# Optimization experiments

Hardware: AMD Instinct MI355X
Metric: run time of the kernel (lower is better)

Reference implementation:

```python
import jax, jax.numpy as jnp
import numpy as np

HIDDEN = 768
NUM_BLOCKS = 8
BLOCK = HIDDEN // NUM_BLOCKS  # 96
FACTOR = 1
LAMBDA = 0.01  # sparsity_threshold
HTF = 1.0      # hard_thresholding_fraction
SCALE = 0.02


def setup_inputs() -> dict:
    key = jax.random.key(0)
    kx, k1, k2, k3, k4 = jax.random.split(key, 5)
    B, H, W = 2, 256, 256
    x = jax.random.normal(kx, (B, HIDDEN, H, W), dtype=jnp.float32)
    w1 = SCALE * jax.random.normal(k1, (NUM_BLOCKS, BLOCK, BLOCK * FACTOR, 2), dtype=jnp.float32)
    b1 = SCALE * jax.random.normal(k2, (NUM_BLOCKS, BLOCK * FACTOR, 1, 1, 2), dtype=jnp.float32)
    w2 = SCALE * jax.random.normal(k3, (NUM_BLOCKS, BLOCK * FACTOR, BLOCK, 2), dtype=jnp.float32)
    b2 = SCALE * jax.random.normal(k4, (NUM_BLOCKS, BLOCK, 1, 1, 2), dtype=jnp.float32)
    return {"x": x, "w1": w1, "b1": b1, "w2": w2, "b2": b2}


def _compl_mul_add(a, w, c):
    # a: (b,k,i,x,y,2) real/imag pairs; w: (k,i,o,2); c: (k,o,1,1,2)
    ar, ai = a[..., 0], a[..., 1]
    wr, wi = w[..., 0], w[..., 1]
    rr = jnp.einsum('bkixy,kio->bkoxy', ar, wr)
    ii = jnp.einsum('bkixy,kio->bkoxy', ai, wi)
    ir = jnp.einsum('bkixy,kio->bkoxy', ai, wr)
    ri = jnp.einsum('bkixy,kio->bkoxy', ar, wi)
    return jnp.stack([rr - ii, ir + ri], axis=-1) + c


def _softshrink(x, lam):
    return jnp.where(x > lam, x - lam, jnp.where(x < -lam, x + lam, jnp.zeros_like(x)))


def reference(x, w1, b1, w2, b2):
    B, C, H, W = x.shape
    total_modes = H // 2 + 1
    kept = int(total_modes * HTF)
    bias = x
    xf = jnp.fft.rfft2(x, s=(H, W), axes=(-2, -1), norm='ortho')  # (B,C,H,W//2+1)
    xf = xf.reshape(B, NUM_BLOCKS, BLOCK, H, W // 2 + 1)
    xr = jnp.stack([jnp.real(xf), jnp.imag(xf)], axis=-1)  # view_as_real
    lo, hi = total_modes - kept, total_modes + kept
    o1 = jax.nn.relu(_compl_mul_add(xr[:, :, :, lo:hi, :kept, :], w1, b1))
    o2 = jnp.zeros_like(xr).at[:, :, :, lo:hi, :kept, :].set(_compl_mul_add(o1, w2, b2))
    s = _softshrink(o2, LAMBDA)
    xc = (s[..., 0] + 1j * s[..., 1]).reshape(B, C, H, W // 2 + 1)
    out = jnp.fft.irfft2(xc, s=(H, W), axes=(-2, -1), norm='ortho').astype(x.dtype)
    return out + bias
```

## Files before the change

kernel.cpp:

```cpp
#include <hip/hip_runtime.h>
#include <hip/hip_bf16.h>
#include <math.h>


#define LAMBDA_SS 0.01f

typedef unsigned int u32;
typedef __attribute__((ext_vector_type(8))) short bf16x8;
typedef __attribute__((ext_vector_type(4))) float f32x4;

__device__ __forceinline__ u32 pack_bf16(float r, float i) {
  union { float f; u32 u; } ur, ui;
  ur.f = r; ui.f = i;
  u32 rb = (ur.u + 0x7FFFu + ((ur.u >> 16) & 1u)) >> 16;
  u32 ib = (ui.u + 0x7FFFu + ((ui.u >> 16) & 1u)) >> 16;
  return (ib << 16) | (rb & 0xFFFFu);
}

__device__ __forceinline__ float2 unpack_bf16(u32 p) {
  union { u32 u; float f; } a, b;
  a.u = (p & 0xFFFFu) << 16;
  b.u = (p & 0xFFFF0000u);
  return make_float2(a.f, b.f);
}

__device__ __forceinline__ float sshrink(float v) {
  return (v > LAMBDA_SS) ? v - LAMBDA_SS : ((v < -LAMBDA_SS) ? v + LAMBDA_SS : 0.f);
}

__device__ __forceinline__ float2 cadd(float2 a, float2 b){ return make_float2(a.x+b.x, a.y+b.y); }
__device__ __forceinline__ float2 csub(float2 a, float2 b){ return make_float2(a.x-b.x, a.y-b.y); }
__device__ __forceinline__ float2 cmul(float2 a, float2 b){
  return make_float2(fmaf(a.x,b.x,-a.y*b.y), fmaf(a.x,b.y,a.y*b.x));
}
__device__ __forceinline__ float2 cmulj(float2 a, float si){
  return make_float2(-si*a.y, si*a.x);
}
__device__ __forceinline__ float2 shflx(float2 v, int m){
  return make_float2(__shfl_xor(v.x, m, 64), __shfl_xor(v.y, m, 64));
}
__device__ __forceinline__ float2 shfll(float2 v, int l){
  return make_float2(__shfl(v.x, l, 64), __shfl(v.y, l, 64));
}
__device__ __forceinline__ int brev6(int x){ return (int)(__brev((u32)x) >> 26); }

struct Tw { float2 t128, t64, t32, t16, t8, t4; float si; };

__device__ __forceinline__ float2 mkTw(int e, float si){
  float a = (float)e * 0.0245436926f;
  return make_float2(cosf(a), si*sinf(a));
}
__device__ __forceinline__ Tw make_tw(int lane, float si){
  Tw w; w.si = si;
  w.t128 = mkTw(lane, si);
  w.t64  = mkTw(2*lane, si);
  w.t32  = mkTw((lane&31)*4, si);
  w.t16  = mkTw((lane&15)*8, si);
  w.t8   = mkTw((lane&7)*16, si);
  w.t4   = mkTw((lane&3)*32, si);
  return w;
}

__device__ __forceinline__ float2 bfly_dif(float2 v, int h, float2 th, int lane){
  float2 p = shflx(v, h);
  float sx = (lane & h) ? -1.f : 1.f;
  float2 s = make_float2(fmaf(sx, v.x, p.x), fmaf(sx, v.y, p.y));
  if (lane & h) s = cmul(s, th);
  return s;
}
__device__ __forceinline__ float2 bfly_dit(float2 v, int h, float2 th, int lane){
  if (lane & h) v = cmul(v, th);
  float2 p = shflx(v, h);
  float sx = (lane & h) ? -1.f : 1.f;
  return make_float2(fmaf(sx, v.x, p.x), fmaf(sx, v.y, p.y));
}

__device__ __forceinline__ void fft256_dif(float2 v[4], int lane, const Tw& T){
  float2 t128b = cmulj(T.t128, T.si);
  { float2 a=v[0], b=v[2]; v[0]=cadd(a,b); v[2]=cmul(csub(a,b), T.t128);
    float2 c=v[1], d=v[3]; v[1]=cadd(c,d); v[3]=cmul(csub(c,d), t128b); }
  { float2 a=v[0], b=v[1]; v[0]=cadd(a,b); v[1]=cmul(csub(a,b), T.t64);
    float2 c=v[2], d=v[3]; v[2]=cadd(c,d); v[3]=cmul(csub(c,d), T.t64); }
#pragma unroll
  for (int r=0;r<4;++r) v[r]=bfly_dif(v[r],32,T.t32,lane);
#pragma unroll
  for (int r=0;r<4;++r) v[r]=bfly_dif(v[r],16,T.t16,lane);
#pragma unroll
  for (int r=0;r<4;++r) v[r]=bfly_dif(v[r],8,T.t8,lane);
#pragma unroll
  for (int r=0;r<4;++r) v[r]=bfly_dif(v[r],4,T.t4,lane);
#pragma unroll
  for (int r=0;r<4;++r){
    float2 p=shflx(v[r],2);
    float sx=(lane&2)?-1.f:1.f;
    float2 s=make_float2(fmaf(sx,v[r].x,p.x), fmaf(sx,v[r].y,p.y));
    if ((lane&3)==3) s=cmulj(s,T.si);
    v[r]=s;
  }
#pragma unroll
  for (int r=0;r<4;++r){
    float2 p=shflx(v[r],1);
    float sx=(lane&1)?-1.f:1.f;
    v[r]=make_float2(fmaf(sx,v[r].x,p.x), fmaf(sx,v[r].y,p.y));
  }
}

__device__ __forceinline__ void fft256_dit(float2 v[4], int lane, const Tw& T){
#pragma unroll
  for (int r=0;r<4;++r){
    float2 p=shflx(v[r],1);
    float sx=(lane&1)?-1.f:1.f;
    v[r]=make_float2(fmaf(sx,v[r].x,p.x), fmaf(sx,v[r].y,p.y));
  }
#pragma unroll
  for (int r=0;r<4;++r){
    float2 w=v[r];
    if ((lane&3)==3) w=cmulj(w,T.si);
    float2 p=shflx(w,2);
    float sx=(lane&2)?-1.f:1.f;
    v[r]=make_float2(fmaf(sx,w.x,p.x), fmaf(sx,w.y,p.y));
  }
#pragma unroll
  for (int r=0;r<4;++r) v[r]=bfly_dit(v[r],4,T.t4,lane);
#pragma unroll
  for (int r=0;r<4;++r) v[r]=bfly_dit(v[r],8,T.t8,lane);
#pragma unroll
  for (int r=0;r<4;++r) v[r]=bfly_dit(v[r],16,T.t16,lane);
#pragma unroll
  for (int r=0;r<4;++r) v[r]=bfly_dit(v[r],32,T.t32,lane);
  { v[1]=cmul(v[1],T.t64); float2 a=v[0]; v[0]=cadd(a,v[1]); v[1]=csub(a,v[1]);
    v[3]=cmul(v[3],T.t64); float2 c=v[2]; v[2]=cadd(c,v[3]); v[3]=csub(c,v[3]); }
  { v[2]=cmul(v[2],T.t128); v[3]=cmul(v[3], cmulj(T.t128,T.si));
    float2 a=v[0]; v[0]=cadd(a,v[2]); v[2]=csub(a,v[2]);
    float2 b=v[1]; v[1]=cadd(b,v[3]); v[3]=csub(b,v[3]); }
}

__device__ __forceinline__ int stage_row(int kw){ return 33*(kw&3) + (kw>>2); }

__global__ __launch_bounds__(256) void k_rowfft(const float* __restrict__ x, u32* __restrict__ F) {
  __shared__ u32 stage[131*65];
  const int bc = blockIdx.x >> 2, hc = blockIdx.x & 3;
  const int tid = threadIdx.x, wave = tid >> 6, lane = tid & 63;
  Tw T = make_tw(lane, -1.f);
  const int L = brev6(lane);
  const int laneP0 = brev6((64 - L) & 63);
  const int lanePX = 63 - lane;

  for (int rr = 0; rr < 8; ++rr) {
    const int hl0 = wave*16 + rr*2, hl1 = hl0 + 1;
    const float* xa = x + ((size_t)bc*256 + hc*64 + hl0) * 256;
    float2 v[4];
#pragma unroll
    for (int r=0;r<4;++r){ int d = lane + 64*r; v[r] = make_float2(xa[d], xa[256+d]); }
    fft256_dif(v, lane, T);
#define UNSCR(R, RP, C, LP) { \
      float2 z = v[R]; float2 p = shfll(v[RP], LP); \
      float2 A  = make_float2(0.5f*(z.x+p.x), 0.5f*(z.y-p.y)); \
      float2 Bv = make_float2(0.5f*(z.y+p.y), 0.5f*(p.x-z.x)); \
      int kw = 4*L + (C); \
      if (kw <= 128) { int row = stage_row(kw); \
        stage[row*65 + hl0] = pack_bf16(A.x, A.y); \
        stage[row*65 + hl1] = pack_bf16(Bv.x, Bv.y); } }
    UNSCR(0, 0, 0, laneP0)
    UNSCR(1, 1, 2, lanePX)
    UNSCR(2, 3, 1, lanePX)
    UNSCR(3, 2, 3, lanePX)
#undef UNSCR
  }
  __syncthreads();
  for (int idx = tid; idx < 129*64; idx += 256) {
    int kw = idx >> 6, hl = idx & 63;
    F[((size_t)bc*129 + kw)*256 + hc*64 + hl] = stage[stage_row(kw)*65 + hl];
  }
}

__global__ __launch_bounds__(256) void k_colfft(u32* __restrict__ F, int inverse) {
  const int tid = threadIdx.x, wave = tid >> 6, lane = tid & 63;
  const float si = inverse ? 1.f : -1.f;
  Tw T = make_tw(lane, si);
  u32* p = F + ((size_t)blockIdx.x*4 + wave) * 256;
  float2 v[4];
#pragma unroll
  for (int r=0;r<4;++r) v[r] = unpack_bf16(p[lane + 64*r]);
  if (!inverse) fft256_dif(v, lane, T);
  else          fft256_dit(v, lane, T);
  const float s = 1.0f/256.0f;
#pragma unroll
  for (int r=0;r<4;++r) p[lane + 64*r] = pack_bf16(v[r].x*s, v[r].y*s);
}

__global__ __launch_bounds__(256) void k_prep_w(const float2* __restrict__ w1,
                                                const float2* __restrict__ w2,
                                                u32* __restrict__ Wt) {
  const int blk = blockIdx.x;
  const int k = blk >> 1, layer = blk & 1;
  const float2* w = (layer == 0 ? w1 : w2) + (size_t)k * 96 * 96;
  u32* out = Wt + (size_t)blk * 18432;
  for (int idx = threadIdx.x; idx < 9216; idx += 256) {
    int o = idx % 96, i = idx / 96;
    float2 v = w[i * 96 + o];
    out[(2 * o) * 96 + i]     = pack_bf16(v.x, -v.y);
    out[(2 * o + 1) * 96 + i] = pack_bf16(v.y, v.x);
  }
}

#define MIX_LDS_BYTES (73728 + 49152)

__global__ __launch_bounds__(512) void k_mix_mfma(u32* __restrict__ F,
    const u32* __restrict__ Wt,
    const float2* __restrict__ b1, const float2* __restrict__ b2) {
  extern __shared__ char smem[];
  char* Wlds = smem;
  char* Dlds = smem + 73728;

  const int bi = blockIdx.x;
  const int hc = bi & 1;
  const int kw = (bi >> 1) % 129;
  const int bk = (bi >> 1) / 129;
  const int k = bk & 7, b = bk >> 3;
  const int t = threadIdx.x;
  const int lane = t & 63, wave = t >> 6;
  const int wm = wave >> 2, wn = wave & 3;
  const int lrow = lane & 15;
  const int lk = (lane >> 4) * 16;

  const u32* W1g = Wt + (size_t)(k * 2 + 0) * 18432;
  const u32* W2g = Wt + (size_t)(k * 2 + 1) * 18432;

#pragma unroll
  for (int c = 0; c < 9; ++c) {
    int idx = c * 512 + t;
    int byte = idx * 16;
    int row = idx / 24;
    uint4 v = reinterpret_cast<const uint4*>(W1g)[idx];
    *reinterpret_cast<uint4*>(Wlds + (byte ^ ((row & 7) << 4))) = v;
  }

  const size_t chstride = 129 * 256;
  const size_t base = (((size_t)(b * 768 + k * 96)) * 129 + kw) * 256 + (size_t)hc * 128;
  {
    const int h = t & 127;
    const int pg = t >> 7;
#pragma unroll
    for (int it = 0; it < 12; ++it) {
      int p = it * 4 + pg;
      u32 a0 = F[base + (size_t)(2 * p) * chstride + h];
      u32 a1 = F[base + (size_t)(2 * p + 1) * chstride + h];
      int byte = h * 384 + p * 8;
      *reinterpret_cast<uint2*>(Dlds + (byte ^ ((h & 7) << 4))) = make_uint2(a0, a1);
    }
  }

  uint4 w2buf[9];
#pragma unroll
  for (int c = 0; c < 9; ++c) w2buf[c] = reinterpret_cast<const uint4*>(W2g)[c * 512 + t];

  __syncthreads();

  f32x4 acc[6][2];
#pragma unroll
  for (int mi = 0; mi < 6; ++mi)
#pragma unroll
    for (int ni = 0; ni < 2; ++ni) acc[mi][ni] = (f32x4)0.f;

#pragma unroll
  for (int ks = 0; ks < 6; ++ks) {
    const int kb = ks * 64;
    bf16x8 afrag[6];
#pragma unroll
    for (int mi = 0; mi < 6; ++mi) {
      int row = wm * 96 + mi * 16 + lrow;
      int byte = row * 384 + kb + lk;
      afrag[mi] = *reinterpret_cast<bf16x8*>(Wlds + (byte ^ ((row & 7) << 4)));
    }
#pragma unroll
    for (int ni = 0; ni < 2; ++ni) {
      int row = wn * 32 + ni * 16 + lrow;
      int byte = row * 384 + kb + lk;
      bf16x8 bfrag = *reinterpret_cast<bf16x8*>(Dlds + (byte ^ ((row & 7) << 4)));
#pragma unroll
      for (int mi = 0; mi < 6; ++mi)
        acc[mi][ni] = __builtin_amdgcn_mfma_f32_16x16x32_bf16(afrag[mi], bfrag, acc[mi][ni], 0, 0, 0);
    }
  }
  __syncthreads();

#pragma unroll
  for (int c = 0; c < 9; ++c) {
    int idx = c * 512 + t;
    int byte = idx * 16;
    int row = idx / 24;
    *reinterpret_cast<uint4*>(Wlds + (byte ^ ((row & 7) << 4))) = w2buf[c];
  }
  const float2* b1k = b1 + k * 96;
#pragma unroll
  for (int mi = 0; mi < 6; ++mi) {
    int m0 = wm * 96 + mi * 16 + 4 * (lane >> 4);
    int o0 = m0 >> 1;
    float2 ba = b1k[o0], bb = b1k[o0 + 1];
#pragma unroll
    for (int ni = 0; ni < 2; ++ni) {
      int n = wn * 32 + ni * 16 + lrow;
      f32x4 v = acc[mi][ni];
      u32 lo  = pack_bf16(fmaxf(v[0] + ba.x, 0.f), fmaxf(v[1] + ba.y, 0.f));
      u32 hi  = pack_bf16(fmaxf(v[2] + bb.x, 0.f), fmaxf(v[3] + bb.y, 0.f));
      int byte = n * 384 + m0 * 2;
      *reinterpret_cast<uint2*>(Dlds + (byte ^ ((n & 7) << 4))) = make_uint2(lo, hi);
    }
  }
  __syncthreads();

#pragma unroll
  for (int mi = 0; mi < 6; ++mi)
#pragma unroll
    for (int ni = 0; ni < 2; ++ni) acc[mi][ni] = (f32x4)0.f;

#pragma unroll
  for (int ks = 0; ks < 6; ++ks) {
    const int kb = ks * 64;
    bf16x8 afrag[6];
#pragma unroll
    for (int mi = 0; mi < 6; ++mi) {
      int row = wm * 96 + mi * 16 + lrow;
      int byte = row * 384 + kb + lk;
      afrag[mi] = *reinterpret_cast<bf16x8*>(Wlds + (byte ^ ((row & 7) << 4)));
    }
#pragma unroll
    for (int ni = 0; ni < 2; ++ni) {
      int row = wn * 32 + ni * 16 + lrow;
      int byte = row * 384 + kb + lk;
      bf16x8 bfrag = *reinterpret_cast<bf16x8*>(Dlds + (byte ^ ((row & 7) << 4)));
#pragma unroll
      for (int mi = 0; mi < 6; ++mi)
        acc[mi][ni] = __builtin_amdgcn_mfma_f32_16x16x32_bf16(afrag[mi], bfrag, acc[mi][ni], 0, 0, 0);
    }
  }

  const float2* b2k = b2 + k * 96;
#pragma unroll
  for (int mi = 0; mi < 6; ++mi) {
    int m0 = wm * 96 + mi * 16 + 4 * (lane >> 4);
    int o0 = m0 >> 1;
    float2 ca = b2k[o0], cb = b2k[o0 + 1];
#pragma unroll
    for (int ni = 0; ni < 2; ++ni) {
      int n = wn * 32 + ni * 16 + lrow;
      f32x4 v = acc[mi][ni];
      u32 lo = pack_bf16(sshrink(v[0] + ca.x), sshrink(v[1] + ca.y));
      u32 hi = pack_bf16(sshrink(v[2] + cb.x), sshrink(v[3] + cb.y));
      F[base + (size_t)o0 * chstride + n]       = lo;
      F[base + (size_t)(o0 + 1) * chstride + n] = hi;
    }
  }
}

__global__ __launch_bounds__(256) void k_rowifft(const u32* __restrict__ F,
                                                 const float* __restrict__ x,
                                                 float* __restrict__ out) {
  __shared__ u32 stage[131*65];
  const int bc = blockIdx.x >> 2, hc = blockIdx.x & 3;
  const int tid = threadIdx.x, wave = tid >> 6, lane = tid & 63;
  Tw T = make_tw(lane, 1.f);
  for (int idx = tid; idx < 129*64; idx += 256) {
    int kw = idx >> 6, hl = idx & 63;
    stage[stage_row(kw)*65 + hl] = F[((size_t)bc*129 + kw)*256 + hc*64 + hl];
  }
  __syncthreads();

  const int L = brev6(lane);
  for (int rr = 0; rr < 8; ++rr) {
    const int hl0 = wave*16 + rr*2, hl1 = hl0 + 1;
    float2 v[4];
#pragma unroll
    for (int r=0;r<4;++r) {
      int c = ((r&1)<<1) | (r>>1);
      int kw = 4*L + c;
      int src = (kw <= 128) ? kw : 256 - kw;
      float sg = (kw <= 128) ? 1.f : -1.f;
      int row = stage_row(src);
      float2 a = unpack_bf16(stage[row*65 + hl0]);
      float2 b = unpack_bf16(stage[row*65 + hl1]);
      a.y *= sg; b.y *= sg;
      if (kw == 0 || kw == 128) { a.y = 0.f; b.y = 0.f; }
      v[r] = make_float2(a.x - b.y, a.y + b.x);
    }
    fft256_dit(v, lane, T);
    const float* xa = x   + ((size_t)bc*256 + hc*64 + hl0) * 256;
    float*       oa = out + ((size_t)bc*256 + hc*64 + hl0) * 256;
#pragma unroll
    for (int r=0;r<4;++r) {
      int d = lane + 64*r;
      oa[d]       = v[r].x + xa[d];
      oa[256 + d] = v[r].y + xa[256 + d];
    }
  }
}

extern "C" void kernel_launch(void* const* d_in, const int* in_sizes, int n_in,
                              void* d_out, int out_size, void* d_ws, size_t ws_size,
                              hipStream_t stream) {
  const float* x   = (const float*)d_in[0];
  const float2* w1 = (const float2*)d_in[1];
  const float2* b1 = (const float2*)d_in[2];
  const float2* w2 = (const float2*)d_in[3];
  const float2* b2 = (const float2*)d_in[4];
  float* out = (float*)d_out;
  u32* F = (u32*)d_ws;
  u32* Wt = (u32*)d_out;

  (void)hipFuncSetAttribute(reinterpret_cast<const void*>(k_mix_mfma),
                            hipFuncAttributeMaxDynamicSharedMemorySize, MIX_LDS_BYTES);

  const int n_rows_blocks = 1536 * 4;
  const int n_cols_blocks = (1536 * 129) / 4;
  const int n_mix_blocks  = 2 * 8 * 129 * 2;

  k_prep_w<<<16, 256, 0, stream>>>(w1, w2, Wt);
  k_rowfft<<<n_rows_blocks, 256, 0, stream>>>(x, F);
  k_colfft<<<n_cols_blocks, 256, 0, stream>>>(F, 0);
  k_mix_mfma<<<n_mix_blocks, 512, MIX_LDS_BYTES, stream>>>(F, Wt, b1, b2);
  k_colfft<<<n_cols_blocks, 256, 0, stream>>>(F, 1);
  k_rowifft<<<n_rows_blocks, 256, 0, stream>>>(F, x, out);
}
```

Measured before the change: 886.1 us.

## Fuse column FFTs with spectral MLP mixing into one kernel

Merges the forward column FFT, the two complex MFMA layers, and the inverse column FFT into a single kernel. Each block now handles a full 256-long column set for one (b, block, kw) triple, so the intermediate spectrum stays in LDS instead of making two extra global round trips. Weights are read directly from global or L2 into registers with double-buffered prefetch instead of being staged in LDS. The block index is remapped to group blocks that share the same weight block. This raises per-thread register pressure (raw[12][4] and a 6x4 accumulator) and halves the grid size, which may reduce occupancy.

After: 908.7 us. +2.5%, slower.

```diff
diff --git a/kernel.cpp b/kernel.cpp
--- a/kernel.cpp
+++ b/kernel.cpp
@@ -174,21 +174,6 @@
   }
 }
 
-__global__ __launch_bounds__(256) void k_colfft(u32* __restrict__ F, int inverse) {
-  const int tid = threadIdx.x, wave = tid >> 6, lane = tid & 63;
-  const float si = inverse ? 1.f : -1.f;
-  Tw T = make_tw(lane, si);
-  u32* p = F + ((size_t)blockIdx.x*4 + wave) * 256;
-  float2 v[4];
-#pragma unroll
-  for (int r=0;r<4;++r) v[r] = unpack_bf16(p[lane + 64*r]);
-  if (!inverse) fft256_dif(v, lane, T);
-  else          fft256_dit(v, lane, T);
-  const float s = 1.0f/256.0f;
-#pragma unroll
-  for (int r=0;r<4;++r) p[lane + 64*r] = pack_bf16(v[r].x*s, v[r].y*s);
-}
-
 __global__ __launch_bounds__(256) void k_prep_w(const float2* __restrict__ w1,
                                                 const float2* __restrict__ w2,
                                                 u32* __restrict__ Wt) {
@@ -204,108 +189,107 @@
   }
 }
 
-#define MIX_LDS_BYTES (73728 + 49152)
-
-__global__ __launch_bounds__(512) void k_mix_mfma(u32* __restrict__ F,
+#define CM_LDS_BYTES 99072
+
+__global__ __launch_bounds__(512, 2) void k_colmix(u32* __restrict__ F,
     const u32* __restrict__ Wt,
     const float2* __restrict__ b1, const float2* __restrict__ b2) {
   extern __shared__ char smem[];
-  char* Wlds = smem;
-  char* Dlds = smem + 73728;
-
-  const int bi = blockIdx.x;
-  const int hc = bi & 1;
-  const int kw = (bi >> 1) % 129;
-  const int bk = (bi >> 1) / 129;
+
+  const int bi = (blockIdx.x & 7) * 258 + (blockIdx.x >> 3);
+  const int kw = bi % 129;
+  const int bk = bi / 129;
   const int k = bk & 7, b = bk >> 3;
   const int t = threadIdx.x;
   const int lane = t & 63, wave = t >> 6;
   const int wm = wave >> 2, wn = wave & 3;
   const int lrow = lane & 15;
-  const int lk = (lane >> 4) * 16;
-
-  const u32* W1g = Wt + (size_t)(k * 2 + 0) * 18432;
-  const u32* W2g = Wt + (size_t)(k * 2 + 1) * 18432;
-
-#pragma unroll
-  for (int c = 0; c < 9; ++c) {
-    int idx = c * 512 + t;
-    int byte = idx * 16;
-    int row = idx / 24;
-    uint4 v = reinterpret_cast<const uint4*>(W1g)[idx];
-    *reinterpret_cast<uint4*>(Wlds + (byte ^ ((row & 7) << 4))) = v;
-  }
+  const int g = lane >> 4;
+  const int lk = g * 16;
 
   const size_t chstride = 129 * 256;
-  const size_t base = (((size_t)(b * 768 + k * 96)) * 129 + kw) * 256 + (size_t)hc * 128;
-  {
-    const int h = t & 127;
-    const int pg = t >> 7;
-#pragma unroll
-    for (int it = 0; it < 12; ++it) {
-      int p = it * 4 + pg;
-      u32 a0 = F[base + (size_t)(2 * p) * chstride + h];
-      u32 a1 = F[base + (size_t)(2 * p + 1) * chstride + h];
-      int byte = h * 384 + p * 8;
-      *reinterpret_cast<uint2*>(Dlds + (byte ^ ((h & 7) << 4))) = make_uint2(a0, a1);
-    }
-  }
-
-  uint4 w2buf[9];
-#pragma unroll
-  for (int c = 0; c < 9; ++c) w2buf[c] = reinterpret_cast<const uint4*>(W2g)[c * 512 + t];
-
-  __syncthreads();
-
-  f32x4 acc[6][2];
+  const size_t colbase = (((size_t)(b*768 + k*96)) * 129 + kw) * 256;
+
+  {
+    Tw Tf = make_tw(lane, -1.f);
+    u32 raw[12][4];
+#pragma unroll
+    for (int cc = 0; cc < 12; ++cc) {
+      const u32* p = F + colbase + (size_t)(wave*12 + cc) * chstride;
+#pragma unroll
+      for (int r = 0; r < 4; ++r) raw[cc][r] = p[lane + 64*r];
+    }
+    const float s = 1.f/256.f;
+#pragma unroll
+    for (int cc = 0; cc < 12; ++cc) {
+      float2 v[4];
+#pragma unroll
+      for (int r = 0; r < 4; ++r) v[r] = unpack_bf16(raw[cc][r]);
+      fft256_dif(v, lane, Tf);
+      const int c = wave*12 + cc;
+#pragma unroll
+      for (int r = 0; r < 4; ++r) {
+        int n = lane + 64*r;
+        int byte = n*384 + c*4;
+        *reinterpret_cast<u32*>(smem + (byte ^ ((n&7)<<4))) = pack_bf16(v[r].x*s, v[r].y*s);
+      }
+    }
+  }
+  __syncthreads();
+
+  const bf16x8* W1v = reinterpret_cast<const bf16x8*>(Wt + (size_t)(k*2 + 0) * 18432);
+  const bf16x8* W2v = reinterpret_cast<const bf16x8*>(Wt + (size_t)(k*2 + 1) * 18432);
+
+  f32x4 acc[6][4];
+
 #pragma unroll
   for (int mi = 0; mi < 6; ++mi)
 #pragma unroll
-    for (int ni = 0; ni < 2; ++ni) acc[mi][ni] = (f32x4)0.f;
-
-#pragma unroll
-  for (int ks = 0; ks < 6; ++ks) {
-    const int kb = ks * 64;
-    bf16x8 afrag[6];
+    for (int ni = 0; ni < 4; ++ni) acc[mi][ni] = (f32x4)0.f;
+  {
+    bf16x8 af[2][6];
+#pragma unroll
+    for (int mi = 0; mi < 6; ++mi)
+      af[0][mi] = W1v[(wm*96 + mi*16 + lrow)*24 + g];
+#pragma unroll
+    for (int ks = 0; ks < 6; ++ks) {
+      if (ks < 5) {
+#pragma unroll
+        for (int mi = 0; mi < 6; ++mi)
+          af[(ks+1)&1][mi] = W1v[(wm*96 + mi*16 + lrow)*24 + (ks+1)*4 + g];
+      }
+      bf16x8 bf[4];
+#pragma unroll
+      for (int ni = 0; ni < 4; ++ni) {
+        int n = wn*64 + ni*16 + lrow;
+        int byte = n*384 + ks*64 + lk;
+        bf[ni] = *reinterpret_cast<bf16x8*>(smem + (byte ^ ((n&7)<<4)));
+      }
+#pragma unroll
+      for (int ni = 0; ni < 4; ++ni)
+#pragma unroll
+        for (int mi = 0; mi < 6; ++mi)
+          acc[mi][ni] = __builtin_amdgcn_mfma_f32_16x16x32_bf16(af[ks&1][mi], bf[ni], acc[mi][ni], 0, 0, 0);
+    }
+  }
+  __syncthreads();
+
+  {
+    const float2* b1k = b1 + k * 96;
 #pragma unroll
     for (int mi = 0; mi < 6; ++mi) {
-      int row = wm * 96 + mi * 16 + lrow;
-      int byte = row * 384 + kb + lk;
-      afrag[mi] = *reinterpret_cast<bf16x8*>(Wlds + (byte ^ ((row & 7) << 4)));
-    }
-#pragma unroll
-    for (int ni = 0; ni < 2; ++ni) {
-      int row = wn * 32 + ni * 16 + lrow;
-      int byte = row * 384 + kb + lk;
-      bf16x8 bfrag = *reinterpret_cast<bf16x8*>(Dlds + (byte ^ ((row & 7) << 4)));
-#pragma unroll
-      for (int mi = 0; mi < 6; ++mi)
-        acc[mi][ni] = __builtin_amdgcn_mfma_f32_16x16x32_bf16(afrag[mi], bfrag, acc[mi][ni], 0, 0, 0);
-    }
-  }
-  __syncthreads();
-
-#pragma unroll
-  for (int c = 0; c < 9; ++c) {
-    int idx = c * 512 + t;
-    int byte = idx * 16;
-    int row = idx / 24;
-    *reinterpret_cast<uint4*>(Wlds + (byte ^ ((row & 7) << 4))) = w2buf[c];
-  }
-  const float2* b1k = b1 + k * 96;
-#pragma unroll
-  for (int mi = 0; mi < 6; ++mi) {
-    int m0 = wm * 96 + mi * 16 + 4 * (lane >> 4);
-    int o0 = m0 >> 1;
-    float2 ba = b1k[o0], bb = b1k[o0 + 1];
-#pragma unroll
-    for (int ni = 0; ni < 2; ++ni) {
-      int n = wn * 32 + ni * 16 + lrow;
-      f32x4 v = acc[mi][ni];
-      u32 lo  = pack_bf16(fmaxf(v[0] + ba.x, 0.f), fmaxf(v[1] + ba.y, 0.f));
-      u32 hi  = pack_bf16(fmaxf(v[2] + bb.x, 0.f), fmaxf(v[3] + bb.y, 0.f));
-      int byte = n * 384 + m0 * 2;
-      *reinterpret_cast<uint2*>(Dlds + (byte ^ ((n & 7) << 4))) = make_uint2(lo, hi);
+      int m0 = wm*96 + mi*16 + 4*g;
+      int o0 = m0 >> 1;
+      float2 ba = b1k[o0], bb = b1k[o0 + 1];
+#pragma unroll
+      for (int ni = 0; ni < 4; ++ni) {
+        int n = wn*64 + ni*16 + lrow;
+        f32x4 v = acc[mi][ni];
+        u32 lo = pack_bf16(fmaxf(v[0] + ba.x, 0.f), fmaxf(v[1] + ba.y, 0.f));
+        u32 hi = pack_bf16(fmaxf(v[2] + bb.x, 0.f), fmaxf(v[3] + bb.y, 0.f));
+        int byte = n*384 + m0*2;
+        *reinterpret_cast<uint2*>(smem + (byte ^ ((n&7)<<4))) = make_uint2(lo, hi);
+      }
     }
   }
   __syncthreads();
@@ -313,43 +297,68 @@
 #pragma unroll
   for (int mi = 0; mi < 6; ++mi)
 #pragma unroll
-    for (int ni = 0; ni < 2; ++ni) acc[mi][ni] = (f32x4)0.f;
-
-#pragma unroll
-  for (int ks = 0; ks < 6; ++ks) {
-    const int kb = ks * 64;
-    bf16x8 afrag[6];
+    for (int ni = 0; ni < 4; ++ni) acc[mi][ni] = (f32x4)0.f;
+  {
+    bf16x8 af[2][6];
+#pragma unroll
+    for (int mi = 0; mi < 6; ++mi)
+      af[0][mi] = W2v[(wm*96 + mi*16 + lrow)*24 + g];
+#pragma unroll
+    for (int ks = 0; ks < 6; ++ks) {
+      if (ks < 5) {
+#pragma unroll
+        for (int mi = 0; mi < 6; ++mi)
+          af[(ks+1)&1][mi] = W2v[(wm*96 + mi*16 + lrow)*24 + (ks+1)*4 + g];
+      }
+      bf16x8 bf[4];
+#pragma unroll
+      for (int ni = 0; ni < 4; ++ni) {
+        int n = wn*64 + ni*16 + lrow;
+        int byte = n*384 + ks*64 + lk;
+        bf[ni] = *reinterpret_cast<bf16x8*>(smem + (byte ^ ((n&7)<<4)));
+      }
+#pragma unroll
+      for (int ni = 0; ni < 4; ++ni)
+#pragma unroll
+        for (int mi = 0; mi < 6; ++mi)
+          acc[mi][ni] = __builtin_amdgcn_mfma_f32_16x16x32_bf16(af[ks&1][mi], bf[ni], acc[mi][ni], 0, 0, 0);
+    }
+  }
+  __syncthreads();
+
+  {
+    u32* Clds = reinterpret_cast<u32*>(smem);
+    const float2* b2k = b2 + k * 96;
 #pragma unroll
     for (int mi = 0; mi < 6; ++mi) {
-      int row = wm * 96 + mi * 16 + lrow;
-      int byte = row * 384 + kb + lk;
-      afrag[mi] = *reinterpret_cast<bf16x8*>(Wlds + (byte ^ ((row & 7) << 4)));
-    }
-#pragma unroll
-    for (int ni = 0; ni < 2; ++ni) {
-      int row = wn * 32 + ni * 16 + lrow;
-      int byte = row * 384 + kb + lk;
-      bf16x8 bfrag = *reinterpret_cast<bf16x8*>(Dlds + (byte ^ ((row & 7) << 4)));
-#pragma unroll
-      for (int mi = 0; mi < 6; ++mi)
-        acc[mi][ni] = __builtin_amdgcn_mfma_f32_16x16x32_bf16(afrag[mi], bfrag, acc[mi][ni], 0, 0, 0);
-    }
-  }
-
-  const float2* b2k = b2 + k * 96;
-#pragma unroll
-  for (int mi = 0; mi < 6; ++mi) {
-    int m0 = wm * 96 + mi * 16 + 4 * (lane >> 4);
-    int o0 = m0 >> 1;
-    float2 ca = b2k[o0], cb = b2k[o0 + 1];
-#pragma unroll
-    for (int ni = 0; ni < 2; ++ni) {
-      int n = wn * 32 + ni * 16 + lrow;
-      f32x4 v = acc[mi][ni];
-      u32 lo = pack_bf16(sshrink(v[0] + ca.x), sshrink(v[1] + ca.y));
-      u32 hi = pack_bf16(sshrink(v[2] + cb.x), sshrink(v[3] + cb.y));
-      F[base + (size_t)o0 * chstride + n]       = lo;
-      F[base + (size_t)(o0 + 1) * chstride + n] = hi;
+      int m0 = wm*96 + mi*16 + 4*g;
+      int o0 = m0 >> 1;
+      float2 ca = b2k[o0], cb = b2k[o0 + 1];
+#pragma unroll
+      for (int ni = 0; ni < 4; ++ni) {
+        int n = wn*64 + ni*16 + lrow;
+        f32x4 v = acc[mi][ni];
+        Clds[o0*258 + n]       = pack_bf16(sshrink(v[0] + ca.x), sshrink(v[1] + ca.y));
+        Clds[(o0 + 1)*258 + n] = pack_bf16(sshrink(v[2] + cb.x), sshrink(v[3] + cb.y));
+      }
+    }
+  }
+  __syncthreads();
+
+  {
+    const u32* Clds = reinterpret_cast<const u32*>(smem);
+    Tw Ti = make_tw(lane, 1.f);
+    const float s = 1.f/256.f;
+#pragma unroll
+    for (int cc = 0; cc < 12; ++cc) {
+      const int c = wave*12 + cc;
+      float2 v[4];
+#pragma unroll
+      for (int r = 0; r < 4; ++r) v[r] = unpack_bf16(Clds[c*258 + lane + 64*r]);
+      fft256_dit(v, lane, Ti);
+      u32* p = F + colbase + (size_t)c * chstride;
+#pragma unroll
+      for (int r = 0; r < 4; ++r) p[lane + 64*r] = pack_bf16(v[r].x*s, v[r].y*s);
     }
   }
 }
@@ -408,17 +417,14 @@
   u32* F = (u32*)d_ws;
   u32* Wt = (u32*)d_out;
 
-  (void)hipFuncSetAttribute(reinterpret_cast<const void*>(k_mix_mfma),
-                            hipFuncAttributeMaxDynamicSharedMemorySize, MIX_LDS_BYTES);
+  (void)hipFuncSetAttribute(reinterpret_cast<const void*>(k_colmix),
+                            hipFuncAttributeMaxDynamicSharedMemorySize, CM_LDS_BYTES);
 
   const int n_rows_blocks = 1536 * 4;
-  const int n_cols_blocks = (1536 * 129) / 4;
-  const int n_mix_blocks  = 2 * 8 * 129 * 2;
+  const int n_cm_blocks   = 2 * 8 * 129;
 
   k_prep_w<<<16, 256, 0, stream>>>(w1, w2, Wt);
   k_rowfft<<<n_rows_blocks, 256, 0, stream>>>(x, F);
-  k_colfft<<<n_cols_blocks, 256, 0, stream>>>(F, 0);
-  k_mix_mfma<<<n_mix_blocks, 512, MIX_LDS_BYTES, stream>>>(F, Wt, b1, b2);
-  k_colfft<<<n_cols_blocks, 256, 0, stream>>>(F, 1);
+  k_colmix<<<n_cm_blocks, 512, CM_LDS_BYTES, stream>>>(F, Wt, b1, b2);
   k_rowifft<<<n_rows_blocks, 256, 0, stream>>>(F, x, out);
 }
```
